# Kernel optimization log

Measured on AMD Instinct MI355X. Metric: run time of the kernel, lower is better.

## Reference

```python
import jax, jax.numpy as jnp
import numpy as np
from jax import lax

B, T, D, H, O = 32, 512, 512, 1024, 512


def setup_inputs() -> dict:
    key = jax.random.key(0)
    ks = jax.random.split(key, 7)
    s = lambda fan_in: 1.0 / np.sqrt(fan_in)
    return {
        "x": jax.random.normal(ks[0], (B, T, D), jnp.float32),
        "Wx0": jax.random.normal(ks[1], (D, 4 * H), jnp.float32) * s(D),
        "Wh0": jax.random.normal(ks[2], (H, 4 * H), jnp.float32) * s(H),
        "b0": jnp.zeros((4 * H,), jnp.float32),
        "Wx1": jax.random.normal(ks[3], (H, 4 * H), jnp.float32) * s(H),
        "Wh1": jax.random.normal(ks[4], (H, 4 * H), jnp.float32) * s(H),
        "b1": jnp.zeros((4 * H,), jnp.float32),
        "Wd": jax.random.normal(ks[5], (H, O), jnp.float32) * s(H),
        "bd": jnp.zeros((O,), jnp.float32),
    }


def _lstm_cell(c, h, inp, Wx, Wh, b):
    # flax OptimizedLSTMCell: fused gate GEMM, gate order i, f, g, o
    z = inp @ Wx + h @ Wh + b  # [B, 4H]
    i, f, g, o = jnp.split(z, 4, axis=-1)
    c_new = jax.nn.sigmoid(f) * c + jax.nn.sigmoid(i) * jnp.tanh(g)
    h_new = jax.nn.sigmoid(o) * jnp.tanh(c_new)
    return c_new, h_new


def reference(x, Wx0, Wh0, b0, Wx1, Wh1, b1, Wd, bd):
    b = x.shape[0]
    h = Wh0.shape[0]
    zero = jnp.zeros((b, h), x.dtype)
    carry0 = ((zero, zero), (zero, zero))  # ((c0, h0), (c1, h1)), zeros like flax default

    def step(carry, xt):
        (c0, h0), (c1, h1) = carry
        c0, h0 = _lstm_cell(c0, h0, xt, Wx0, Wh0, b0)
        c1, h1 = _lstm_cell(c1, h1, h0, Wx1, Wh1, b1)
        return ((c0, h0), (c1, h1)), h1

    xs = jnp.swapaxes(x, 0, 1)  # [T, B, D] for scan over time
    _, ys = lax.scan(step, carry0, xs)
    y = jnp.swapaxes(ys, 0, 1)  # [B, T, H]
    return y @ Wd + bd  # [B, T, O]
```

## Files before the change

kernel.cpp:

```cpp
#include <hip/hip_runtime.h>


typedef _Float16 half8  __attribute__((ext_vector_type(8)));
typedef float    floatx4 __attribute__((ext_vector_type(4)));

#define WREC_OFF   0UL
#define WX0_OFF    25165824UL
#define WD_OFF     29360128UL
#define XH_OFF     30408704UL
#define ZX0_OFF    47185920UL
#define H1_OFF     181403648UL
#define H0_OFF     214958080UL
#define FLAGS_OFF  248512512UL

__device__ __forceinline__ float fsig(float x){ return 1.0f/(1.0f + __expf(-x)); }
__device__ __forceinline__ float ftanhf(float x){
  float e = __expf(2.0f*fabsf(x));
  float r = 1.0f - 2.0f/(e + 1.0f);
  return copysignf(r, x);
}

__global__ void conv_wrec(const float* __restrict__ Wh0,
                          const float* __restrict__ Wx1,
                          const float* __restrict__ Wh1,
                          _Float16* __restrict__ out){
  int idx = blockIdx.x*256 + threadIdx.x;
  if (idx >= 256*3*128*16) return;
  int c  = idx & 15;
  int t1 = idx >> 4;
  int kc = t1 & 127;
  int t2 = t1 >> 7;
  int mat = t2 % 3;
  int wg  = t2 / 3;
  const float* W = (mat==0) ? Wh0 : (mat==1) ? Wx1 : Wh1;
  int col = (c>>2)*1024 + wg*4 + (c&3);
  _Float16* o = out + (size_t)idx*8;
  #pragma unroll
  for (int j=0;j<8;++j) o[j] = (_Float16)W[(kc*8+j)*4096 + col];
}

__global__ void conv_wx0(const float* __restrict__ W, _Float16* __restrict__ out){
  int idx = blockIdx.x*256 + threadIdx.x;
  if (idx >= 256*64*16) return;
  int c  = idx & 15;
  int kc = (idx >> 4) & 63;
  int wg = idx >> 10;
  int col = (c>>2)*1024 + wg*4 + (c&3);
  _Float16* o = out + (size_t)idx*8;
  #pragma unroll
  for (int j=0;j<8;++j) o[j] = (_Float16)W[(kc*8+j)*4096 + col];
}

__global__ void conv_wd(const float* __restrict__ W, _Float16* __restrict__ out){
  int idx = blockIdx.x*256 + threadIdx.x;
  if (idx >= 32*128*16) return;
  int c  = idx & 15;
  int kc = (idx >> 4) & 127;
  int nt = idx >> 11;
  int col = nt*16 + c;
  _Float16* o = out + (size_t)idx*8;
  #pragma unroll
  for (int j=0;j<8;++j) o[j] = (_Float16)W[(kc*8+j)*512 + col];
}

__global__ void conv_x(const float* __restrict__ x, _Float16* __restrict__ xh){
  int idx = blockIdx.x*256 + threadIdx.x;
  if (idx >= 2097152) return;
  int dq = idx & 127;
  int bt = idx >> 7;
  int b  = bt & 31;
  int t  = bt >> 5;
  float4 v = ((const float4*)x)[(size_t)(b*512 + t)*128 + dq];
  _Float16* o = xh + (size_t)idx*4;
  o[0]=(_Float16)v.x; o[1]=(_Float16)v.y; o[2]=(_Float16)v.z; o[3]=(_Float16)v.w;
}

__global__ __launch_bounds__(64) void zx0_gemm(const _Float16* __restrict__ xh,
                                               const _Float16* __restrict__ wx0a,
                                               const float* __restrict__ b0,
                                               _Float16* __restrict__ zx0){
  int t   = blockIdx.x;
  int wgg = blockIdx.y;
  int l = threadIdx.x, q = l>>4, c = l&15;
  floatx4 acc[2][4];
  #pragma unroll
  for (int g=0; g<4; ++g){
    int wg = wgg*4+g;
    float bv = b0[(c>>2)*1024 + wg*4 + (c&3)];
    acc[0][g] = (floatx4){bv,bv,bv,bv};
    acc[1][g] = (floatx4){bv,bv,bv,bv};
  }
  #pragma unroll 4
  for (int ks=0; ks<16; ++ks){
    int kc = ks*4 + q;
    half8 a0 = *(const half8*)(xh + (t*32      + c)*512 + kc*8);
    half8 a1 = *(const half8*)(xh + (t*32 + 16 + c)*512 + kc*8);
    #pragma unroll
    for (int g=0; g<4; ++g){
      int wg = wgg*4+g;
      half8 b = *(const half8*)(wx0a + ((size_t)(wg*64 + kc)*16 + c)*8);
      acc[0][g] = __builtin_amdgcn_mfma_f32_16x16x32_f16(a0,b,acc[0][g],0,0,0);
      acc[1][g] = __builtin_amdgcn_mfma_f32_16x16x32_f16(a1,b,acc[1][g],0,0,0);
    }
  }
  #pragma unroll
  for (int g=0; g<4; ++g){
    int wg = wgg*4+g;
    #pragma unroll
    for (int mt=0; mt<2; ++mt)
      #pragma unroll
      for (int r=0;r<4;++r){
        int m = mt*16 + q*4 + r;
        zx0[((size_t)(t*256 + wg)*32 + m)*16 + c] = (_Float16)acc[mt][g][r];
      }
  }
}

#define AF(base, ks)  (*(const half8*)((base) + (ks)*32))
#define BF(w, ks)     (*(const half8*)((w) + (((ks)*4 + q)*16 + c)*8))

__device__ __forceinline__ void gates_store(floatx4 acc, float* cs,
    _Float16* dst, int g, int c, int mt, int q, int wg){
  #pragma unroll
  for (int r=0;r<4;++r){
    float v0 = acc[r];
    float v1 = __shfl_xor(v0, 4, 64);
    float v2 = __shfl_xor(v0, 8, 64);
    float v3 = __shfl_xor(v1, 8, 64);
    float zi = (g==0)?v0:(g==1)?v1:(g==2)?v2:v3;
    float zf = (g==0)?v1:(g==1)?v0:(g==2)?v3:v2;
    float zg = (g==0)?v2:(g==1)?v3:(g==2)?v0:v1;
    float zo = (g==0)?v3:(g==1)?v2:(g==2)?v1:v0;
    float cn = fsig(zf)*cs[r] + fsig(zi)*ftanhf(zg);
    cs[r] = cn;
    float hv = fsig(zo)*ftanhf(cn);
    unsigned hb16 = (unsigned)__builtin_bit_cast(unsigned short, (_Float16)hv);
    unsigned up   = (unsigned)__shfl_xor((int)hb16, 1, 64);
    if (g==0 && (c&1)==0)
      __hip_atomic_store((unsigned*)(dst + (mt*16 + q*4 + r)*1024 + wg*4 + c),
                         hb16 | (up<<16),
                         __ATOMIC_RELAXED, __HIP_MEMORY_SCOPE_AGENT);
  }
}

__global__ __launch_bounds__(128, 1) void lstm_persist(
    const _Float16* __restrict__ wrec, const _Float16* __restrict__ zx0,
    const float* __restrict__ b1g, _Float16* __restrict__ h0a,
    _Float16* __restrict__ h1a, unsigned int* __restrict__ flags)
{
  extern __shared__ _Float16 lds[];
  _Float16* w0  = lds;
  _Float16* w1  = lds + 16384;
  _Float16* w2  = lds + 32768;

  const int wg = blockIdx.x, tid = threadIdx.x;
  const int wv = tid>>6, l = tid&63, q = l>>4, c = l&15;
  const int g = (c>>2);
  const int mt = wv;
  const int row = mt*16 + c;
  const int grp = wg >> 3;

  unsigned int* gcnt = flags + grp*64;
  unsigned int* root = flags + 2048;
  unsigned int* go   = flags + 4096;

  {
    const uint4* src = (const uint4*)(wrec + (size_t)wg*49152);
    uint4* dst = (uint4*)lds;
    for (int i=tid; i<6144; i+=128) dst[i] = src[i];
  }
  float c0[4] = {0,0,0,0}, c1[4] = {0,0,0,0};
  const float b1v = b1g[g*1024 + wg*4 + (c&3)];
  __syncthreads();

  {
    const _Float16* zsrc = zx0 + ((size_t)wg*32 + mt*16 + q*4)*16 + c;
    floatx4 a;
    a[0]=(float)zsrc[0]; a[1]=(float)zsrc[16]; a[2]=(float)zsrc[32]; a[3]=(float)zsrc[48];
    gates_store(a, c0, h0a, g, c, mt, q, wg);
  }

  for (int t=0; t<512; ++t){
    int tn = (t<511) ? t+1 : 511;
    const _Float16* zsrc = zx0 + ((size_t)(tn*256 + wg)*32 + mt*16 + q*4)*16 + c;
    float pz0=(float)zsrc[0], pz1=(float)zsrc[16], pz2=(float)zsrc[32], pz3=(float)zsrc[48];

    __syncthreads();
    if (tid==0){
      unsigned tgt = (unsigned)(t+1);
      unsigned o = __hip_atomic_fetch_add(gcnt, 1u, __ATOMIC_RELAXED,
                                          __HIP_MEMORY_SCOPE_AGENT);
      if (o == 8u*tgt - 1u){
        unsigned r = __hip_atomic_fetch_add(root, 1u, __ATOMIC_RELAXED,
                                            __HIP_MEMORY_SCOPE_AGENT);
        if (r == 32u*tgt - 1u){
          #pragma unroll
          for (int g2=0; g2<32; ++g2)
            __hip_atomic_store(go + g2*64, tgt, __ATOMIC_RELAXED,
                               __HIP_MEMORY_SCOPE_AGENT);
        }
      }
      while (__hip_atomic_load(go + grp*64, __ATOMIC_RELAXED,
                               __HIP_MEMORY_SCOPE_AGENT) < tgt)
        __builtin_amdgcn_s_sleep(1);
    }
    __syncthreads();

    const _Float16* h0c = h0a + (size_t)t*32768 + row*1024 + q*8;
    const _Float16* h1p = h1a + (size_t)(t-1)*32768 + row*1024 + q*8;
    half8 H1[32], H0[32];
    if (t > 0){
      #pragma unroll
      for (int s=0; s<32; ++s) H1[s] = AF(h1p, s);
    }
    #pragma unroll
    for (int s=0; s<32; ++s) H0[s] = AF(h0c, s);

    floatx4 aA0={0,0,0,0}, aA1={0,0,0,0};
    floatx4 aB0={b1v,b1v,b1v,b1v}, aB1={0,0,0,0};
    floatx4 aC0={0,0,0,0}, aC1={0,0,0,0};
    if (t > 0){
      #pragma unroll
      for (int s=0; s<16; ++s){
        aC0 = __builtin_amdgcn_mfma_f32_16x16x32_f16(H1[s],    BF(w2,s),    aC0,0,0,0);
        aC1 = __builtin_amdgcn_mfma_f32_16x16x32_f16(H1[16+s], BF(w2,16+s), aC1,0,0,0);
      }
    }
    #pragma unroll
    for (int s=0; s<16; ++s){
      aB0 = __builtin_amdgcn_mfma_f32_16x16x32_f16(H0[s],    BF(w1,s),    aB0,0,0,0);
      aB1 = __builtin_amdgcn_mfma_f32_16x16x32_f16(H0[16+s], BF(w1,16+s), aB1,0,0,0);
      aA0 = __builtin_amdgcn_mfma_f32_16x16x32_f16(H0[s],    BF(w0,s),    aA0,0,0,0);
      aA1 = __builtin_amdgcn_mfma_f32_16x16x32_f16(H0[16+s], BF(w0,16+s), aA1,0,0,0);
    }
    {
      floatx4 z1 = (aB0+aB1)+(aC0+aC1);
      gates_store(z1, c1, h1a + (size_t)t*32768, g, c, mt, q, wg);
    }
    if (t < 511){
      floatx4 z0 = aA0+aA1;
      z0[0]+=pz0; z0[1]+=pz1; z0[2]+=pz2; z0[3]+=pz3;
      gates_store(z0, c0, h0a + (size_t)(t+1)*32768, g, c, mt, q, wg);
    }
  }
}

__global__ __launch_bounds__(256) void wd_gemm(const _Float16* __restrict__ h1a,
                                               const _Float16* __restrict__ wda,
                                               const float* __restrict__ bd,
                                               float* __restrict__ y){
  int mb = blockIdx.x;
  int nb = blockIdx.y;
  int tid = threadIdx.x, wv = tid>>6, l = tid&63, q = l>>4, c = l&15;
  int mt = wv & 1, nh = wv >> 1;
  floatx4 acc[4];
  #pragma unroll
  for (int gg=0; gg<4; ++gg) acc[gg] = (floatx4){0.f,0.f,0.f,0.f};
  const _Float16* arow = h1a + (size_t)(mb*32 + mt*16 + c)*1024;
  #pragma unroll 4
  for (int ks=0; ks<32; ++ks){
    int kc = ks*4 + q;
    half8 a = *(const half8*)(arow + kc*8);
    #pragma unroll
    for (int gg=0; gg<4; ++gg){
      int nt = nb*8 + nh*4 + gg;
      half8 b = *(const half8*)(wda + ((size_t)(nt*128 + kc)*16 + c)*8);
      acc[gg] = __builtin_amdgcn_mfma_f32_16x16x32_f16(a,b,acc[gg],0,0,0);
    }
  }
  #pragma unroll
  for (int gg=0; gg<4; ++gg){
    int o = nb*128 + nh*64 + gg*16 + c;
    float bdv = bd[o];
    #pragma unroll
    for (int r=0;r<4;++r){
      int row = mb*32 + mt*16 + q*4 + r;
      int tt = row >> 5, bb = row & 31;
      y[(size_t)bb*262144 + tt*512 + o] = acc[gg][r] + bdv;
    }
  }
}

extern "C" void kernel_launch(void* const* d_in, const int* in_sizes, int n_in,
                              void* d_out, int out_size, void* d_ws, size_t ws_size,
                              hipStream_t stream){
  const float* x   = (const float*)d_in[0];
  const float* Wx0 = (const float*)d_in[1];
  const float* Wh0 = (const float*)d_in[2];
  const float* b0  = (const float*)d_in[3];
  const float* Wx1 = (const float*)d_in[4];
  const float* Wh1 = (const float*)d_in[5];
  const float* b1  = (const float*)d_in[6];
  const float* Wd  = (const float*)d_in[7];
  const float* bd  = (const float*)d_in[8];
  float* y = (float*)d_out;
  char* ws = (char*)d_ws;

  _Float16* wrec = (_Float16*)(ws + WREC_OFF);
  _Float16* wx0a = (_Float16*)(ws + WX0_OFF);
  _Float16* wda  = (_Float16*)(ws + WD_OFF);
  _Float16* xh   = (_Float16*)(ws + XH_OFF);
  _Float16* zx0  = (_Float16*)(ws + ZX0_OFF);
  _Float16* h1a  = (_Float16*)(ws + H1_OFF);
  _Float16* h0a  = (_Float16*)(ws + H0_OFF);
  unsigned int* flags = (unsigned int*)(ws + FLAGS_OFF);

  hipMemsetAsync(flags, 0, 24576, stream);
  conv_wrec<<<dim3(6144), dim3(256), 0, stream>>>(Wh0, Wx1, Wh1, wrec);
  conv_wx0 <<<dim3(1024), dim3(256), 0, stream>>>(Wx0, wx0a);
  conv_wd  <<<dim3(256),  dim3(256), 0, stream>>>(Wd, wda);
  conv_x   <<<dim3(8192), dim3(256), 0, stream>>>(x, xh);
  zx0_gemm <<<dim3(512,64), dim3(64), 0, stream>>>(xh, wx0a, b0, zx0);
  hipFuncSetAttribute((const void*)lstm_persist,
                      hipFuncAttributeMaxDynamicSharedMemorySize, 98304);
  lstm_persist<<<dim3(256), dim3(128), 98304, stream>>>(wrec, zx0, b1, h0a, h1a, flags);
  wd_gemm  <<<dim3(512,4), dim3(256), 0, stream>>>(h1a, wda, bd, y);
}
```

Before: 5.113 ms.

## Fuse layer-0 input projection into persistent LSTM kernel, overlapped with barrier wait

Removes the separate zx0_gemm pre-pass and its large fp16 intermediate. Each persistent workgroup now keeps its slice of Wx0 in LDS and computes the x@Wx0 gate contribution for the next timestep itself. That work runs between arriving at the grid barrier and spinning on it, so it can hide inside the wait. The cost is more LDS per block (112 KB) and extra MFMA and x loads on the recurrent critical path whenever the barrier wait is short.

```diff
diff --git a/kernel.cpp b/kernel.cpp
--- a/kernel.cpp
+++ b/kernel.cpp
@@ -8,10 +8,9 @@
 #define WX0_OFF    25165824UL
 #define WD_OFF     29360128UL
 #define XH_OFF     30408704UL
-#define ZX0_OFF    47185920UL
-#define H1_OFF     181403648UL
-#define H0_OFF     214958080UL
-#define FLAGS_OFF  248512512UL
+#define H1_OFF     47185920UL
+#define H0_OFF     80740352UL
+#define FLAGS_OFF  114294784UL
 
 __device__ __forceinline__ float fsig(float x){ return 1.0f/(1.0f + __expf(-x)); }
 __device__ __forceinline__ float ftanhf(float x){
@@ -73,47 +72,6 @@
   float4 v = ((const float4*)x)[(size_t)(b*512 + t)*128 + dq];
   _Float16* o = xh + (size_t)idx*4;
   o[0]=(_Float16)v.x; o[1]=(_Float16)v.y; o[2]=(_Float16)v.z; o[3]=(_Float16)v.w;
-}
-
-__global__ __launch_bounds__(64) void zx0_gemm(const _Float16* __restrict__ xh,
-                                               const _Float16* __restrict__ wx0a,
-                                               const float* __restrict__ b0,
-                                               _Float16* __restrict__ zx0){
-  int t   = blockIdx.x;
-  int wgg = blockIdx.y;
-  int l = threadIdx.x, q = l>>4, c = l&15;
-  floatx4 acc[2][4];
-  #pragma unroll
-  for (int g=0; g<4; ++g){
-    int wg = wgg*4+g;
-    float bv = b0[(c>>2)*1024 + wg*4 + (c&3)];
-    acc[0][g] = (floatx4){bv,bv,bv,bv};
-    acc[1][g] = (floatx4){bv,bv,bv,bv};
-  }
-  #pragma unroll 4
-  for (int ks=0; ks<16; ++ks){
-    int kc = ks*4 + q;
-    half8 a0 = *(const half8*)(xh + (t*32      + c)*512 + kc*8);
-    half8 a1 = *(const half8*)(xh + (t*32 + 16 + c)*512 + kc*8);
-    #pragma unroll
-    for (int g=0; g<4; ++g){
-      int wg = wgg*4+g;
-      half8 b = *(const half8*)(wx0a + ((size_t)(wg*64 + kc)*16 + c)*8);
-      acc[0][g] = __builtin_amdgcn_mfma_f32_16x16x32_f16(a0,b,acc[0][g],0,0,0);
-      acc[1][g] = __builtin_amdgcn_mfma_f32_16x16x32_f16(a1,b,acc[1][g],0,0,0);
-    }
-  }
-  #pragma unroll
-  for (int g=0; g<4; ++g){
-    int wg = wgg*4+g;
-    #pragma unroll
-    for (int mt=0; mt<2; ++mt)
-      #pragma unroll
-      for (int r=0;r<4;++r){
-        int m = mt*16 + q*4 + r;
-        zx0[((size_t)(t*256 + wg)*32 + m)*16 + c] = (_Float16)acc[mt][g][r];
-      }
-  }
 }
 
 #define AF(base, ks)  (*(const half8*)((base) + (ks)*32))
@@ -144,14 +102,17 @@
 }
 
 __global__ __launch_bounds__(128, 1) void lstm_persist(
-    const _Float16* __restrict__ wrec, const _Float16* __restrict__ zx0,
-    const float* __restrict__ b1g, _Float16* __restrict__ h0a,
-    _Float16* __restrict__ h1a, unsigned int* __restrict__ flags)
+    const _Float16* __restrict__ wrec, const _Float16* __restrict__ wx0a,
+    const _Float16* __restrict__ xh,
+    const float* __restrict__ b0g, const float* __restrict__ b1g,
+    _Float16* __restrict__ h0a, _Float16* __restrict__ h1a,
+    unsigned int* __restrict__ flags)
 {
   extern __shared__ _Float16 lds[];
   _Float16* w0  = lds;
   _Float16* w1  = lds + 16384;
   _Float16* w2  = lds + 32768;
+  _Float16* w3  = lds + 49152;
 
   const int wg = blockIdx.x, tid = threadIdx.x;
   const int wv = tid>>6, l = tid&63, q = l>>4, c = l&15;
@@ -165,29 +126,34 @@
   unsigned int* go   = flags + 4096;
 
   {
-    const uint4* src = (const uint4*)(wrec + (size_t)wg*49152);
+    const uint4* srcA = (const uint4*)(wrec + (size_t)wg*49152);
+    const uint4* srcB = (const uint4*)(wx0a + (size_t)wg*8192);
     uint4* dst = (uint4*)lds;
-    for (int i=tid; i<6144; i+=128) dst[i] = src[i];
+    for (int i=tid; i<6144; i+=128) dst[i] = srcA[i];
+    for (int i=tid; i<1024; i+=128) dst[6144+i] = srcB[i];
   }
   float c0[4] = {0,0,0,0}, c1[4] = {0,0,0,0};
+  const float b0v = b0g[g*1024 + wg*4 + (c&3)];
   const float b1v = b1g[g*1024 + wg*4 + (c&3)];
   __syncthreads();
 
   {
-    const _Float16* zsrc = zx0 + ((size_t)wg*32 + mt*16 + q*4)*16 + c;
-    floatx4 a;
-    a[0]=(float)zsrc[0]; a[1]=(float)zsrc[16]; a[2]=(float)zsrc[32]; a[3]=(float)zsrc[48];
-    gates_store(a, c0, h0a, g, c, mt, q, wg);
+    const _Float16* xb = xh + (size_t)row*512 + q*8;
+    floatx4 p0={b0v,b0v,b0v,b0v}, p1={0,0,0,0};
+    #pragma unroll
+    for (int s=0; s<8; ++s){
+      p0 = __builtin_amdgcn_mfma_f32_16x16x32_f16(AF(xb,s),   BF(w3,s),   p0,0,0,0);
+      p1 = __builtin_amdgcn_mfma_f32_16x16x32_f16(AF(xb,8+s), BF(w3,8+s), p1,0,0,0);
+    }
+    floatx4 z = p0+p1;
+    gates_store(z, c0, h0a, g, c, mt, q, wg);
   }
 
   for (int t=0; t<512; ++t){
-    int tn = (t<511) ? t+1 : 511;
-    const _Float16* zsrc = zx0 + ((size_t)(tn*256 + wg)*32 + mt*16 + q*4)*16 + c;
-    float pz0=(float)zsrc[0], pz1=(float)zsrc[16], pz2=(float)zsrc[32], pz3=(float)zsrc[48];
-
     __syncthreads();
+
+    const unsigned tgt = (unsigned)(t+1);
     if (tid==0){
-      unsigned tgt = (unsigned)(t+1);
       unsigned o = __hip_atomic_fetch_add(gcnt, 1u, __ATOMIC_RELAXED,
                                           __HIP_MEMORY_SCOPE_AGENT);
       if (o == 8u*tgt - 1u){
@@ -200,6 +166,21 @@
                                __HIP_MEMORY_SCOPE_AGENT);
         }
       }
+    }
+
+    int tn = (t<511) ? t+1 : 511;
+    const _Float16* xb = xh + (size_t)(tn*32 + row)*512 + q*8;
+    half8 X[16];
+    #pragma unroll
+    for (int s=0; s<16; ++s) X[s] = AF(xb, s);
+    floatx4 aA0={b0v,b0v,b0v,b0v}, aA1={0,0,0,0};
+    #pragma unroll
+    for (int s=0; s<8; ++s){
+      aA0 = __builtin_amdgcn_mfma_f32_16x16x32_f16(X[s],   BF(w3,s),   aA0,0,0,0);
+      aA1 = __builtin_amdgcn_mfma_f32_16x16x32_f16(X[8+s], BF(w3,8+s), aA1,0,0,0);
+    }
+
+    if (tid==0){
       while (__hip_atomic_load(go + grp*64, __ATOMIC_RELAXED,
                                __HIP_MEMORY_SCOPE_AGENT) < tgt)
         __builtin_amdgcn_s_sleep(1);
@@ -216,7 +197,6 @@
     #pragma unroll
     for (int s=0; s<32; ++s) H0[s] = AF(h0c, s);
 
-    floatx4 aA0={0,0,0,0}, aA1={0,0,0,0};
     floatx4 aB0={b1v,b1v,b1v,b1v}, aB1={0,0,0,0};
     floatx4 aC0={0,0,0,0}, aC1={0,0,0,0};
     if (t > 0){
@@ -239,7 +219,6 @@
     }
     if (t < 511){
       floatx4 z0 = aA0+aA1;
-      z0[0]+=pz0; z0[1]+=pz1; z0[2]+=pz2; z0[3]+=pz3;
       gates_store(z0, c0, h0a + (size_t)(t+1)*32768, g, c, mt, q, wg);
     }
   }
@@ -300,7 +279,6 @@
   _Float16* wx0a = (_Float16*)(ws + WX0_OFF);
   _Float16* wda  = (_Float16*)(ws + WD_OFF);
   _Float16* xh   = (_Float16*)(ws + XH_OFF);
-  _Float16* zx0  = (_Float16*)(ws + ZX0_OFF);
   _Float16* h1a  = (_Float16*)(ws + H1_OFF);
   _Float16* h0a  = (_Float16*)(ws + H0_OFF);
   unsigned int* flags = (unsigned int*)(ws + FLAGS_OFF);
@@ -310,9 +288,9 @@
   conv_wx0 <<<dim3(1024), dim3(256), 0, stream>>>(Wx0, wx0a);
   conv_wd  <<<dim3(256),  dim3(256), 0, stream>>>(Wd, wda);
   conv_x   <<<dim3(8192), dim3(256), 0, stream>>>(x, xh);
-  zx0_gemm <<<dim3(512,64), dim3(64), 0, stream>>>(xh, wx0a, b0, zx0);
   hipFuncSetAttribute((const void*)lstm_persist,
-                      hipFuncAttributeMaxDynamicSharedMemorySize, 98304);
-  lstm_persist<<<dim3(256), dim3(128), 98304, stream>>>(wrec, zx0, b1, h0a, h1a, flags);
+                      hipFuncAttributeMaxDynamicSharedMemorySize, 114688);
+  lstm_persist<<<dim3(256), dim3(128), 114688, stream>>>(wrec, wx0a, xh, b0, b1,
+                                                         h0a, h1a, flags);
   wd_gemm  <<<dim3(512,4), dim3(256), 0, stream>>>(h1a, wda, bd, y);
 }
```

After: 5.167 ms. No clear change (+1.1%).

## Prefetch neighbor hidden-state slices into cache while waiting at grid barrier

Applied to the files above, without the earlier changes.

The per-step grid barrier is split across waves. Wave 0 still does the hierarchical arrive. Lanes of the other wave poll per-group counters and, once the producing groups have arrived, issue a dummy global load of their freshly written h0/h1 slices to pull them into cache before the global go-flag is released. The aim is to hide the latency of the h0/h1 loads after the barrier. In exchange it adds extra atomic polling traffic on the flag lines during the wait.

```diff
diff --git a/kernel.cpp b/kernel.cpp
--- a/kernel.cpp
+++ b/kernel.cpp
@@ -159,6 +159,7 @@
   const int mt = wv;
   const int row = mt*16 + c;
   const int grp = wg >> 3;
+  const int slice = (wg >> 3) & 31;
 
   unsigned int* gcnt = flags + grp*64;
   unsigned int* root = flags + 2048;
@@ -186,23 +187,58 @@
     float pz0=(float)zsrc[0], pz1=(float)zsrc[16], pz2=(float)zsrc[32], pz3=(float)zsrc[48];
 
     __syncthreads();
-    if (tid==0){
-      unsigned tgt = (unsigned)(t+1);
-      unsigned o = __hip_atomic_fetch_add(gcnt, 1u, __ATOMIC_RELAXED,
-                                          __HIP_MEMORY_SCOPE_AGENT);
-      if (o == 8u*tgt - 1u){
-        unsigned r = __hip_atomic_fetch_add(root, 1u, __ATOMIC_RELAXED,
+
+    const unsigned tgt = (unsigned)(t+1);
+    if (wv == 0){
+      if (l == 0){
+        unsigned o = __hip_atomic_fetch_add(gcnt, 1u, __ATOMIC_RELAXED,
                                             __HIP_MEMORY_SCOPE_AGENT);
-        if (r == 32u*tgt - 1u){
-          #pragma unroll
-          for (int g2=0; g2<32; ++g2)
-            __hip_atomic_store(go + g2*64, tgt, __ATOMIC_RELAXED,
-                               __HIP_MEMORY_SCOPE_AGENT);
+        if (o == 8u*tgt - 1u){
+          unsigned r = __hip_atomic_fetch_add(root, 1u, __ATOMIC_RELAXED,
+                                              __HIP_MEMORY_SCOPE_AGENT);
+          if (r == 32u*tgt - 1u){
+            #pragma unroll
+            for (int g2=0; g2<32; ++g2)
+              __hip_atomic_store(go + g2*64, tgt, __ATOMIC_RELAXED,
+                                 __HIP_MEMORY_SCOPE_AGENT);
+          }
         }
       }
-      while (__hip_atomic_load(go + grp*64, __ATOMIC_RELAXED,
-                               __HIP_MEMORY_SCOPE_AGENT) < tgt)
+    } else {
+      const _Float16* tp = nullptr;
+      const unsigned int *ga = nullptr, *gb = nullptr;
+      if (l >= 1 && l <= 16){
+        int w = l-1;
+        tp = h0a + (size_t)t*32768 + slice*1024 + w*64;
+        ga = flags + (2*w)*64; gb = flags + (2*w+1)*64;
+      } else if (l >= 17 && l <= 32 && t > 0){
+        int w = l-17;
+        tp = h1a + (size_t)(t-1)*32768 + slice*1024 + w*64;
+        ga = flags + (2*w)*64; gb = flags + (2*w+1)*64;
+      }
+      const unsigned thr = 8u*tgt;
+      int done = (tp == nullptr);
+      for (;;){
+        int gov = 0;
+        if (l == 0)
+          gov = (int)(__hip_atomic_load(go + grp*64, __ATOMIC_RELAXED,
+                                        __HIP_MEMORY_SCOPE_AGENT) >= tgt);
+        if (!done){
+          unsigned a = __hip_atomic_load(ga, __ATOMIC_RELAXED,
+                                         __HIP_MEMORY_SCOPE_AGENT);
+          unsigned b = __hip_atomic_load(gb, __ATOMIC_RELAXED,
+                                         __HIP_MEMORY_SCOPE_AGENT);
+          if (a >= thr && b >= thr){
+            unsigned tv;
+            asm volatile("global_load_dword %0, %1, off\n\t"
+                         "s_waitcnt vmcnt(0)"
+                         : "=v"(tv) : "v"(tp) : "memory");
+            done = 1;
+          }
+        }
+        if (__shfl(gov, 0, 64)) break;
         __builtin_amdgcn_s_sleep(1);
+      }
     }
     __syncthreads();
 
```

Result: slower. 5.515 ms (+7.9%).
